# Optimization experiments

Measured on AMD Instinct MI355X. Metric: run time of the kernel, lower is better.

## Reference

```python
import jax, jax.numpy as jnp
import numpy as np

N_NODES = 50000
N_EDGES = 800000
D = 128


def gcn_conv(x, src, dst, W, b, num_nodes):
    # PyG GCNConv: h = X W; add self-loops; symmetric deg^-1/2 normalization; scatter-add; + bias
    h = x @ W                                   # [N, F_out]
    ones = jnp.ones(src.shape[0], dtype=h.dtype)
    deg = jax.ops.segment_sum(ones, dst, num_segments=num_nodes)  # in-degree incl. self-loops
    dinv = jax.lax.rsqrt(jnp.maximum(deg, 1.0))  # deg >= 1 because of self-loops
    norm = dinv[src] * dinv[dst]                 # [E+N]
    msg = h[src] * norm[:, None]                 # gather + scale
    out = jax.ops.segment_sum(msg, dst, num_segments=num_nodes)
    return out + b


def setup_inputs() -> dict:
    key = jax.random.key(0)
    ks = jax.random.split(key, 6)
    x = jax.random.normal(ks[0], (N_NODES, D), dtype=jnp.float32)
    edge_index = jax.random.randint(ks[1], (2, N_EDGES), 0, N_NODES, dtype=jnp.int64)
    s = 1.0 / np.sqrt(D)
    W1 = jax.random.normal(ks[2], (D, D), dtype=jnp.float32) * s
    W2 = jax.random.normal(ks[3], (D, D), dtype=jnp.float32) * s
    Wg = jax.random.normal(ks[4], (2 * D, D), dtype=jnp.float32) * (1.0 / np.sqrt(2 * D))
    b1 = jnp.zeros((D,), jnp.float32)
    b2 = jnp.zeros((D,), jnp.float32)
    bg = jnp.zeros((D,), jnp.float32)
    return {"x": x, "edge_index": edge_index, "W1": W1, "b1": b1,
            "W2": W2, "b2": b2, "Wg": Wg, "bg": bg}


def reference(x, edge_index, W1, b1, W2, b2, Wg, bg):
    num_nodes = x.shape[0]
    x0 = jnp.clip(x, -100.0, 100.0)
    loop = jnp.arange(num_nodes, dtype=edge_index.dtype)
    src = jnp.concatenate([edge_index[0], loop])
    dst = jnp.concatenate([edge_index[1], loop])
    h = jax.nn.relu(gcn_conv(x0, src, dst, W1, b1, num_nodes))
    # F.dropout(p=0.3, training=False) -> identity at inference
    h = jax.nn.relu(gcn_conv(h, src, dst, W2, b2, num_nodes))
    h = h + x0  # residual (out_channels == in_channels)
    gate = jax.nn.sigmoid(jnp.concatenate([h, x0], axis=1) @ Wg + bg)
    return h * gate
```

## Files before the change

### kernel.cpp

```cpp
#include <hip/hip_runtime.h>
#include <hip/hip_bf16.h>

using short8 = __attribute__((ext_vector_type(8))) short;
using f32x4  = __attribute__((ext_vector_type(4))) float;

static constexpr int NN = 50000;
static constexpr int NE = 800000;
static constexpr int MPAD = 50048;
static constexpr int NB2 = 256;
static constexpr int BNODE = 196;
static constexpr int CAPB = 4096;
static constexpr int NCHB = 200;
static constexpr int CHB = NE / NCHB;

__device__ __forceinline__ float clip100(float v) { return fminf(fmaxf(v, -100.f), 100.f); }
__device__ __forceinline__ unsigned short f2b(float v) {
    __hip_bfloat16 h = __float2bfloat16(v);
    return *reinterpret_cast<unsigned short*>(&h);
}
__device__ __forceinline__ float blo(unsigned int u) { return __uint_as_float(u << 16); }
__device__ __forceinline__ float bhi(unsigned int u) { return __uint_as_float(u & 0xFFFF0000u); }
__device__ __forceinline__ float b2f(unsigned short u) {
    return __uint_as_float(((unsigned int)u) << 16);
}

__global__ __launch_bounds__(256) void k_bucket(const int* __restrict__ idx,
                                                int2* __restrict__ epair,
                                                int* __restrict__ gcur) {
    __shared__ int ls[CHB], ld[CHB];
    __shared__ int bcnt[NB2], bb[NB2], bofs[NB2];
    const int tid = threadIdx.x;
    const int beg = blockIdx.x * CHB;
    for (int i = tid; i < CHB; i += 256) {
        ls[i] = idx[beg + i];
        ld[i] = idx[NE + beg + i];
    }
    bcnt[tid] = 0;
    __syncthreads();
    for (int i = tid; i < CHB; i += 256) atomicAdd(&bcnt[ld[i] / BNODE], 1);
    __syncthreads();
    bb[tid] = atomicAdd(&gcur[tid], bcnt[tid]);
    bofs[tid] = 0;
    __syncthreads();
    for (int i = tid; i < CHB; i += 256) {
        const int d = ld[i];
        const int p = d / BNODE;
        const int pos = atomicAdd(&bofs[p], 1);
        epair[p * CAPB + bb[p] + pos] = make_int2(ls[i], d);
    }
}

__global__ __launch_bounds__(256) void k_sortfill(const int2* __restrict__ epair,
                                                  const int* __restrict__ gcur,
                                                  int* __restrict__ rowptr,
                                                  float* __restrict__ dinv,
                                                  int* __restrict__ esrc) {
    __shared__ int ls[CAPB], ld[CAPB], srt[CAPB];
    __shared__ int cntL[256], sc[256], cur[256];
    const int t = threadIdx.x;
    const int b = blockIdx.x;
    sc[t] = gcur[t];
    __syncthreads();
    for (int off = 1; off < 256; off <<= 1) {
        const int add = (t >= off) ? sc[t - off] : 0;
        __syncthreads();
        sc[t] += add;
        __syncthreads();
    }
    const int ne = gcur[b];
    const int base = sc[b] - ne;
    const int nb0 = b * BNODE;
    const int nn = min(NN - nb0, BNODE);
    if (b == 0 && t == 0) rowptr[NN] = NE;

    for (int i = t; i < ne; i += 256) {
        const int2 p = epair[b * CAPB + i];
        ls[i] = p.x;
        ld[i] = p.y - nb0;
    }
    cntL[t] = 0;
    __syncthreads();
    for (int i = t; i < ne; i += 256) atomicAdd(&cntL[ld[i]], 1);
    __syncthreads();
    sc[t] = cntL[t];
    __syncthreads();
    for (int off = 1; off < 256; off <<= 1) {
        const int add = (t >= off) ? sc[t - off] : 0;
        __syncthreads();
        sc[t] += add;
        __syncthreads();
    }
    const int excl = sc[t] - cntL[t];
    cur[t] = excl;
    if (t < nn) {
        rowptr[nb0 + t] = base + excl;
        dinv[nb0 + t] = rsqrtf(1.f + (float)cntL[t]);
    }
    __syncthreads();
    for (int i = t; i < ne; i += 256) {
        const int pos = atomicAdd(&cur[ld[i]], 1);
        srt[pos] = ls[i];
    }
    __syncthreads();
    for (int i = t; i < ne; i += 256) esrc[base + i] = srt[i];
}

__global__ __launch_bounds__(256) void k_cvtw(const float* __restrict__ W1,
                                              const float* __restrict__ W2,
                                              const float* __restrict__ Wg,
                                              unsigned short* __restrict__ Wt1,
                                              unsigned short* __restrict__ Wt2,
                                              unsigned short* __restrict__ Wgt,
                                              int* __restrict__ gcur) {
    const int i = blockIdx.x * 256 + threadIdx.x;
    if (i < NB2) gcur[i] = 0;
    if (i < 16384) {
        const int n = i >> 7, k = i & 127;
        Wt1[i] = f2b(W1[k * 128 + n]);
    } else if (i < 32768) {
        const int j = i - 16384;
        const int n = j >> 7, k = j & 127;
        Wt2[j] = f2b(W2[k * 128 + n]);
    } else {
        const int j = i - 32768;
        const int n = j >> 8, k = j & 255;
        Wgt[j] = f2b(Wg[k * 128 + n]);
    }
}

template <bool AB16>
__global__ __launch_bounds__(256) void k_mfma_lds(const unsigned short* __restrict__ Ab,
                                                  const float* __restrict__ Af,
                                                  const unsigned short* __restrict__ Wt,
                                                  unsigned short* __restrict__ Cb,
                                                  const float* __restrict__ dinv) {
    __shared__ unsigned short wl[128 * 136];
    const int tid = threadIdx.x;
#pragma unroll
    for (int j = tid; j < 2048; j += 256) {
        const int row = j >> 4, c8 = j & 15;
        *(short8*)(wl + row * 136 + c8 * 8) = *(const short8*)(Wt + row * 128 + c8 * 8);
    }
    __syncthreads();

    const int wv = tid >> 6;
    const int ln = tid & 63;
    const int l16 = ln & 15;
    const int qd = ln >> 4;
    const int rowb = blockIdx.x * 64 + wv * 16;
    const long arow = rowb + l16;
    const int kq = qd * 8;

    f32x4 acc[8];
#pragma unroll
    for (int i = 0; i < 8; ++i) acc[i] = (f32x4){0.f, 0.f, 0.f, 0.f};

#pragma unroll
    for (int kc = 0; kc < 4; ++kc) {
        short8 a;
        if (AB16) {
            a = *(const short8*)(Ab + arow * 128 + kc * 32 + kq);
        } else {
            a = (short8){0, 0, 0, 0, 0, 0, 0, 0};
            if (arow < NN) {
                const float* fp = Af + arow * 128 + kc * 32 + kq;
                const float4 f0 = *(const float4*)fp;
                const float4 f1 = *(const float4*)(fp + 4);
                a[0] = (short)f2b(clip100(f0.x));
                a[1] = (short)f2b(clip100(f0.y));
                a[2] = (short)f2b(clip100(f0.z));
                a[3] = (short)f2b(clip100(f0.w));
                a[4] = (short)f2b(clip100(f1.x));
                a[5] = (short)f2b(clip100(f1.y));
                a[6] = (short)f2b(clip100(f1.z));
                a[7] = (short)f2b(clip100(f1.w));
            }
        }
#pragma unroll
        for (int nt = 0; nt < 8; ++nt) {
            const short8 b = *(const short8*)(wl + (nt * 16 + l16) * 136 + kc * 32 + kq);
            acc[nt] = __builtin_amdgcn_mfma_f32_16x16x32_bf16(a, b, acc[nt], 0, 0, 0);
        }
    }

    const int r0 = rowb + qd * 4;
#pragma unroll
    for (int r = 0; r < 4; ++r) {
        const int row = r0 + r;
        if (row < NN) {
            const float dv = dinv[row];
#pragma unroll
            for (int nt = 0; nt < 8; ++nt) {
                Cb[(long)row * 128 + nt * 16 + l16] = f2b(acc[nt][r] * dv);
            }
        }
    }
}

__global__ __launch_bounds__(256) void k_mfma_gate(const unsigned short* __restrict__ Ab,
                                                   const float* __restrict__ Af,
                                                   const unsigned short* __restrict__ Wt,
                                                   const float* __restrict__ bg,
                                                   float* __restrict__ out) {
    __shared__ unsigned short wl[128 * 136];
    const int tid = threadIdx.x;
    const int wv = tid >> 6;
    const int ln = tid & 63;
    const int l16 = ln & 15;
    const int qd = ln >> 4;
    const int rowb = blockIdx.x * 64 + wv * 16;
    const long arow = rowb + l16;
    const int kq = qd * 8;

    f32x4 acc[8];
#pragma unroll
    for (int i = 0; i < 8; ++i) acc[i] = (f32x4){0.f, 0.f, 0.f, 0.f};

#pragma unroll
    for (int j = tid; j < 2048; j += 256) {
        const int row = j >> 4, c8 = j & 15;
        *(short8*)(wl + row * 136 + c8 * 8) = *(const short8*)(Wt + row * 256 + c8 * 8);
    }
    __syncthreads();
    {
        const unsigned short* ap = Ab + arow * 128 + kq;
#pragma unroll
        for (int kc = 0; kc < 4; ++kc) {
            const short8 a = *(const short8*)(ap + kc * 32);
#pragma unroll
            for (int nt = 0; nt < 8; ++nt) {
                const short8 b = *(const short8*)(wl + (nt * 16 + l16) * 136 + kc * 32 + kq);
                acc[nt] = __builtin_amdgcn_mfma_f32_16x16x32_bf16(a, b, acc[nt], 0, 0, 0);
            }
        }
    }
    __syncthreads();

#pragma unroll
    for (int j = tid; j < 2048; j += 256) {
        const int row = j >> 4, c8 = j & 15;
        *(short8*)(wl + row * 136 + c8 * 8) = *(const short8*)(Wt + row * 256 + 128 + c8 * 8);
    }
    __syncthreads();
    {
        const bool valid = arow < NN;
        const float* fp = Af + arow * 128 + kq;
#pragma unroll
        for (int kc = 0; kc < 4; ++kc) {
            short8 a = (short8){0, 0, 0, 0, 0, 0, 0, 0};
            if (valid) {
                const float4 f0 = *(const float4*)(fp + kc * 32);
                const float4 f1 = *(const float4*)(fp + kc * 32 + 4);
                a[0] = (short)f2b(clip100(f0.x));
                a[1] = (short)f2b(clip100(f0.y));
                a[2] = (short)f2b(clip100(f0.z));
                a[3] = (short)f2b(clip100(f0.w));
                a[4] = (short)f2b(clip100(f1.x));
                a[5] = (short)f2b(clip100(f1.y));
                a[6] = (short)f2b(clip100(f1.z));
                a[7] = (short)f2b(clip100(f1.w));
            }
#pragma unroll
            for (int nt = 0; nt < 8; ++nt) {
                const short8 b = *(const short8*)(wl + (nt * 16 + l16) * 136 + kc * 32 + kq);
                acc[nt] = __builtin_amdgcn_mfma_f32_16x16x32_bf16(a, b, acc[nt], 0, 0, 0);
            }
        }
    }

    const int r0 = rowb + qd * 4;
#pragma unroll
    for (int nt = 0; nt < 8; ++nt) {
        const int col = nt * 16 + l16;
        const float bgv = bg[col];
#pragma unroll
        for (int r = 0; r < 4; ++r) {
            const int row = r0 + r;
            if (row < NN) {
                const float g = 1.f / (1.f + __expf(-(acc[nt][r] + bgv)));
                out[(long)row * 128 + col] = b2f(Ab[(long)row * 128 + col]) * g;
            }
        }
    }
}

template <bool RES>
__global__ __launch_bounds__(256) void k_aggr(const unsigned int* __restrict__ As2,
                                              unsigned short* __restrict__ Bb,
                                              const int* __restrict__ rowptr,
                                              const int* __restrict__ esrc,
                                              const float* __restrict__ dinv,
                                              const float* __restrict__ bias,
                                              const float* __restrict__ x) {
    const int d = __builtin_amdgcn_readfirstlane((blockIdx.x * 256 + threadIdx.x) >> 6);
    if (d >= NN) return;
    const int lane = threadIdx.x & 63;
    const float dd = dinv[d];

    const unsigned int u = As2[(long)d * 64 + lane];
    float2 acc;
    acc.x = blo(u);
    acc.y = bhi(u);

    const int beg = rowptr[d];
    const int end = rowptr[d + 1];
    int i = beg;
    for (; i + 8 <= end; i += 8) {
        const int s0 = esrc[i + 0], s1 = esrc[i + 1], s2 = esrc[i + 2], s3 = esrc[i + 3];
        const int s4 = esrc[i + 4], s5 = esrc[i + 5], s6 = esrc[i + 6], s7 = esrc[i + 7];
        const unsigned int v0 = As2[(long)s0 * 64 + lane];
        const unsigned int v1 = As2[(long)s1 * 64 + lane];
        const unsigned int v2 = As2[(long)s2 * 64 + lane];
        const unsigned int v3 = As2[(long)s3 * 64 + lane];
        const unsigned int v4 = As2[(long)s4 * 64 + lane];
        const unsigned int v5 = As2[(long)s5 * 64 + lane];
        const unsigned int v6 = As2[(long)s6 * 64 + lane];
        const unsigned int v7 = As2[(long)s7 * 64 + lane];
        acc.x += ((blo(v0) + blo(v1)) + (blo(v2) + blo(v3))) +
                 ((blo(v4) + blo(v5)) + (blo(v6) + blo(v7)));
        acc.y += ((bhi(v0) + bhi(v1)) + (bhi(v2) + bhi(v3))) +
                 ((bhi(v4) + bhi(v5)) + (bhi(v6) + bhi(v7)));
    }
    if (i + 4 <= end) {
        const int s0 = esrc[i + 0], s1 = esrc[i + 1], s2 = esrc[i + 2], s3 = esrc[i + 3];
        const unsigned int v0 = As2[(long)s0 * 64 + lane];
        const unsigned int v1 = As2[(long)s1 * 64 + lane];
        const unsigned int v2 = As2[(long)s2 * 64 + lane];
        const unsigned int v3 = As2[(long)s3 * 64 + lane];
        acc.x += (blo(v0) + blo(v1)) + (blo(v2) + blo(v3));
        acc.y += (bhi(v0) + bhi(v1)) + (bhi(v2) + bhi(v3));
        i += 4;
    }
    for (; i < end; ++i) {
        const unsigned int v = As2[(long)esrc[i] * 64 + lane];
        acc.x += blo(v);
        acc.y += bhi(v);
    }

    const float2 bv = ((const float2*)bias)[lane];
    acc.x = fmaxf(fmaf(acc.x, dd, bv.x), 0.f);
    acc.y = fmaxf(fmaf(acc.y, dd, bv.y), 0.f);
    if (RES) {
        const float2 xv = ((const float2*)x)[(long)d * 64 + lane];
        acc.x += clip100(xv.x);
        acc.y += clip100(xv.y);
    }
    const unsigned int pack = (unsigned int)f2b(acc.x) | ((unsigned int)f2b(acc.y) << 16);
    ((unsigned int*)Bb)[(long)d * 64 + lane] = pack;
}

extern "C" void kernel_launch(void* const* d_in, const int* in_sizes, int n_in,
                              void* d_out, int out_size, void* d_ws, size_t ws_size,
                              hipStream_t stream) {
    const float* x  = (const float*)d_in[0];
    const int*  eix = (const int*)d_in[1];
    const float* W1 = (const float*)d_in[2];
    const float* b1 = (const float*)d_in[3];
    const float* W2 = (const float*)d_in[4];
    const float* b2 = (const float*)d_in[5];
    const float* Wg = (const float*)d_in[6];
    const float* bg = (const float*)d_in[7];
    float* out = (float*)d_out;

    char* ws = (char*)d_ws;
    unsigned short* As   = (unsigned short*)ws;
    unsigned short* hb   = (unsigned short*)(ws + 12812288);
    unsigned short* Wt1  = (unsigned short*)(ws + 25624576);
    unsigned short* Wt2  = (unsigned short*)(ws + 25657344);
    unsigned short* Wgt  = (unsigned short*)(ws + 25690112);
    int*   rowptr = (int*)(ws + 25755648);
    float* dinv   = (float*)(ws + 25956352);
    int*   gcur   = (int*)(ws + 26157056);
    int*   esrc   = (int*)(ws + 26159104);
    int2*  epair  = (int2*)(ws + 29359104);

    const int ggrid = MPAD / 64;
    dim3 blk(256);

    k_cvtw<<<256, blk, 0, stream>>>(W1, W2, Wg, Wt1, Wt2, Wgt, gcur);
    k_bucket<<<NCHB, blk, 0, stream>>>(eix, epair, gcur);
    k_sortfill<<<NB2, blk, 0, stream>>>(epair, gcur, rowptr, dinv, esrc);

    k_mfma_lds<false><<<ggrid, blk, 0, stream>>>(nullptr, x, Wt1, As, dinv);
    k_aggr<false><<<(NN * 64 + 255) / 256, blk, 0, stream>>>(
        (const unsigned int*)As, hb, rowptr, esrc, dinv, b1, nullptr);

    k_mfma_lds<true><<<ggrid, blk, 0, stream>>>(hb, nullptr, Wt2, As, dinv);
    k_aggr<true><<<(NN * 64 + 255) / 256, blk, 0, stream>>>(
        (const unsigned int*)As, hb, rowptr, esrc, dinv, b2, x);

    k_mfma_gate<<<ggrid, blk, 0, stream>>>(hb, x, Wgt, bg, out);
}
```

Baseline: 213.8 us.

## Fuse preprocessing kernels and overlap CSR build with first GEMM

The weight-conversion kernel is merged with edge bucketing, and the CSR sort/fill kernel is merged with the first X·W1 GEMM into one grid. Those two jobs are picked by block index, so the first GEMM no longer waits for the CSR build. To break the GEMM's dependency on dinv, the source-side degree scaling moves into the first aggregation, which now gathers dinv[src] per edge. This removes kernel launches and serialization gaps. In exchange, layer-1 aggregation does extra per-edge loads and multiplies, and the merged kernel needs more shared memory, which may lower occupancy for its GEMM blocks.

```diff
diff --git a/kernel.cpp b/kernel.cpp
--- a/kernel.cpp
+++ b/kernel.cpp
@@ -24,146 +24,143 @@
     return __uint_as_float(((unsigned int)u) << 16);
 }
 
-__global__ __launch_bounds__(256) void k_bucket(const int* __restrict__ idx,
-                                                int2* __restrict__ epair,
-                                                int* __restrict__ gcur) {
+__global__ __launch_bounds__(256) void k_front(const int* __restrict__ idx,
+                                               int2* __restrict__ epair,
+                                               int* __restrict__ gcur,
+                                               const float* __restrict__ W1,
+                                               const float* __restrict__ W2,
+                                               const float* __restrict__ Wg,
+                                               unsigned short* __restrict__ Wt1,
+                                               unsigned short* __restrict__ Wt2,
+                                               unsigned short* __restrict__ Wgt) {
     __shared__ int ls[CHB], ld[CHB];
     __shared__ int bcnt[NB2], bb[NB2], bofs[NB2];
     const int tid = threadIdx.x;
-    const int beg = blockIdx.x * CHB;
-    for (int i = tid; i < CHB; i += 256) {
-        ls[i] = idx[beg + i];
-        ld[i] = idx[NE + beg + i];
-    }
-    bcnt[tid] = 0;
-    __syncthreads();
-    for (int i = tid; i < CHB; i += 256) atomicAdd(&bcnt[ld[i] / BNODE], 1);
-    __syncthreads();
-    bb[tid] = atomicAdd(&gcur[tid], bcnt[tid]);
-    bofs[tid] = 0;
-    __syncthreads();
-    for (int i = tid; i < CHB; i += 256) {
-        const int d = ld[i];
-        const int p = d / BNODE;
-        const int pos = atomicAdd(&bofs[p], 1);
-        epair[p * CAPB + bb[p] + pos] = make_int2(ls[i], d);
-    }
-}
-
-__global__ __launch_bounds__(256) void k_sortfill(const int2* __restrict__ epair,
-                                                  const int* __restrict__ gcur,
-                                                  int* __restrict__ rowptr,
-                                                  float* __restrict__ dinv,
-                                                  int* __restrict__ esrc) {
-    __shared__ int ls[CAPB], ld[CAPB], srt[CAPB];
-    __shared__ int cntL[256], sc[256], cur[256];
-    const int t = threadIdx.x;
-    const int b = blockIdx.x;
-    sc[t] = gcur[t];
-    __syncthreads();
-    for (int off = 1; off < 256; off <<= 1) {
-        const int add = (t >= off) ? sc[t - off] : 0;
-        __syncthreads();
-        sc[t] += add;
-        __syncthreads();
-    }
-    const int ne = gcur[b];
-    const int base = sc[b] - ne;
-    const int nb0 = b * BNODE;
-    const int nn = min(NN - nb0, BNODE);
-    if (b == 0 && t == 0) rowptr[NN] = NE;
-
-    for (int i = t; i < ne; i += 256) {
-        const int2 p = epair[b * CAPB + i];
-        ls[i] = p.x;
-        ld[i] = p.y - nb0;
-    }
-    cntL[t] = 0;
-    __syncthreads();
-    for (int i = t; i < ne; i += 256) atomicAdd(&cntL[ld[i]], 1);
-    __syncthreads();
-    sc[t] = cntL[t];
-    __syncthreads();
-    for (int off = 1; off < 256; off <<= 1) {
-        const int add = (t >= off) ? sc[t - off] : 0;
-        __syncthreads();
-        sc[t] += add;
-        __syncthreads();
-    }
-    const int excl = sc[t] - cntL[t];
-    cur[t] = excl;
-    if (t < nn) {
-        rowptr[nb0 + t] = base + excl;
-        dinv[nb0 + t] = rsqrtf(1.f + (float)cntL[t]);
-    }
-    __syncthreads();
-    for (int i = t; i < ne; i += 256) {
-        const int pos = atomicAdd(&cur[ld[i]], 1);
-        srt[pos] = ls[i];
-    }
-    __syncthreads();
-    for (int i = t; i < ne; i += 256) esrc[base + i] = srt[i];
-}
-
-__global__ __launch_bounds__(256) void k_cvtw(const float* __restrict__ W1,
-                                              const float* __restrict__ W2,
-                                              const float* __restrict__ Wg,
-                                              unsigned short* __restrict__ Wt1,
-                                              unsigned short* __restrict__ Wt2,
-                                              unsigned short* __restrict__ Wgt,
-                                              int* __restrict__ gcur) {
-    const int i = blockIdx.x * 256 + threadIdx.x;
-    if (i < NB2) gcur[i] = 0;
-    if (i < 16384) {
-        const int n = i >> 7, k = i & 127;
-        Wt1[i] = f2b(W1[k * 128 + n]);
-    } else if (i < 32768) {
-        const int j = i - 16384;
-        const int n = j >> 7, k = j & 127;
-        Wt2[j] = f2b(W2[k * 128 + n]);
+    if (blockIdx.x < NCHB) {
+        const int beg = blockIdx.x * CHB;
+        for (int i = tid; i < CHB; i += 256) {
+            ls[i] = idx[beg + i];
+            ld[i] = idx[NE + beg + i];
+        }
+        bcnt[tid] = 0;
+        __syncthreads();
+        for (int i = tid; i < CHB; i += 256) atomicAdd(&bcnt[ld[i] / BNODE], 1);
+        __syncthreads();
+        bb[tid] = atomicAdd(&gcur[tid], bcnt[tid]);
+        bofs[tid] = 0;
+        __syncthreads();
+        for (int i = tid; i < CHB; i += 256) {
+            const int d = ld[i];
+            const int p = d / BNODE;
+            const int pos = atomicAdd(&bofs[p], 1);
+            epair[p * CAPB + bb[p] + pos] = make_int2(ls[i], d);
+        }
     } else {
-        const int j = i - 32768;
-        const int n = j >> 8, k = j & 255;
-        Wgt[j] = f2b(Wg[k * 128 + n]);
-    }
-}
-
-template <bool AB16>
-__global__ __launch_bounds__(256) void k_mfma_lds(const unsigned short* __restrict__ Ab,
-                                                  const float* __restrict__ Af,
-                                                  const unsigned short* __restrict__ Wt,
-                                                  unsigned short* __restrict__ Cb,
-                                                  const float* __restrict__ dinv) {
-    __shared__ unsigned short wl[128 * 136];
+        const int i = (blockIdx.x - NCHB) * 256 + tid;
+        if (i < 16384) {
+            const int n = i >> 7, k = i & 127;
+            Wt1[i] = f2b(W1[k * 128 + n]);
+        } else if (i < 32768) {
+            const int j = i - 16384;
+            const int n = j >> 7, k = j & 127;
+            Wt2[j] = f2b(W2[k * 128 + n]);
+        } else {
+            const int j = i - 32768;
+            const int n = j >> 8, k = j & 255;
+            Wgt[j] = f2b(Wg[k * 128 + n]);
+        }
+    }
+}
+
+__global__ __launch_bounds__(256) void k_mid(const int2* __restrict__ epair,
+                                             const int* __restrict__ gcur,
+                                             int* __restrict__ rowptr,
+                                             float* __restrict__ dinv,
+                                             int* __restrict__ esrc,
+                                             const float* __restrict__ x,
+                                             const unsigned short* __restrict__ Wt,
+                                             unsigned short* __restrict__ Cb) {
+    __shared__ alignas(16) char smem[CAPB * 3 * 4 + 3 * 256 * 4];
     const int tid = threadIdx.x;
-#pragma unroll
-    for (int j = tid; j < 2048; j += 256) {
-        const int row = j >> 4, c8 = j & 15;
-        *(short8*)(wl + row * 136 + c8 * 8) = *(const short8*)(Wt + row * 128 + c8 * 8);
-    }
-    __syncthreads();
-
-    const int wv = tid >> 6;
-    const int ln = tid & 63;
-    const int l16 = ln & 15;
-    const int qd = ln >> 4;
-    const int rowb = blockIdx.x * 64 + wv * 16;
-    const long arow = rowb + l16;
-    const int kq = qd * 8;
-
-    f32x4 acc[8];
-#pragma unroll
-    for (int i = 0; i < 8; ++i) acc[i] = (f32x4){0.f, 0.f, 0.f, 0.f};
-
-#pragma unroll
-    for (int kc = 0; kc < 4; ++kc) {
-        short8 a;
-        if (AB16) {
-            a = *(const short8*)(Ab + arow * 128 + kc * 32 + kq);
-        } else {
-            a = (short8){0, 0, 0, 0, 0, 0, 0, 0};
+    if (blockIdx.x < NB2) {
+        int* ls   = (int*)smem;
+        int* ld   = ls + CAPB;
+        int* srt  = ld + CAPB;
+        int* cntL = srt + CAPB;
+        int* sc   = cntL + 256;
+        int* cur  = sc + 256;
+        const int t = tid;
+        const int b = blockIdx.x;
+        sc[t] = gcur[t];
+        __syncthreads();
+        for (int off = 1; off < 256; off <<= 1) {
+            const int add = (t >= off) ? sc[t - off] : 0;
+            __syncthreads();
+            sc[t] += add;
+            __syncthreads();
+        }
+        const int ne = gcur[b];
+        const int base = sc[b] - ne;
+        const int nb0 = b * BNODE;
+        const int nn = min(NN - nb0, BNODE);
+        if (b == 0 && t == 0) rowptr[NN] = NE;
+
+        for (int i = t; i < ne; i += 256) {
+            const int2 p = epair[b * CAPB + i];
+            ls[i] = p.x;
+            ld[i] = p.y - nb0;
+        }
+        cntL[t] = 0;
+        __syncthreads();
+        for (int i = t; i < ne; i += 256) atomicAdd(&cntL[ld[i]], 1);
+        __syncthreads();
+        sc[t] = cntL[t];
+        __syncthreads();
+        for (int off = 1; off < 256; off <<= 1) {
+            const int add = (t >= off) ? sc[t - off] : 0;
+            __syncthreads();
+            sc[t] += add;
+            __syncthreads();
+        }
+        const int excl = sc[t] - cntL[t];
+        cur[t] = excl;
+        if (t < nn) {
+            rowptr[nb0 + t] = base + excl;
+            dinv[nb0 + t] = rsqrtf(1.f + (float)cntL[t]);
+        }
+        __syncthreads();
+        for (int i = t; i < ne; i += 256) {
+            const int pos = atomicAdd(&cur[ld[i]], 1);
+            srt[pos] = ls[i];
+        }
+        __syncthreads();
+        for (int i = t; i < ne; i += 256) esrc[base + i] = srt[i];
+    } else {
+        unsigned short* wl = (unsigned short*)smem;
+#pragma unroll
+        for (int j = tid; j < 2048; j += 256) {
+            const int row = j >> 4, c8 = j & 15;
+            *(short8*)(wl + row * 136 + c8 * 8) = *(const short8*)(Wt + row * 128 + c8 * 8);
+        }
+        __syncthreads();
+
+        const int wv = tid >> 6;
+        const int ln = tid & 63;
+        const int l16 = ln & 15;
+        const int qd = ln >> 4;
+        const int rowb = (blockIdx.x - NB2) * 64 + wv * 16;
+        const long arow = rowb + l16;
+        const int kq = qd * 8;
+
+        f32x4 acc[8];
+#pragma unroll
+        for (int i = 0; i < 8; ++i) acc[i] = (f32x4){0.f, 0.f, 0.f, 0.f};
+
+#pragma unroll
+        for (int kc = 0; kc < 4; ++kc) {
+            short8 a = (short8){0, 0, 0, 0, 0, 0, 0, 0};
             if (arow < NN) {
-                const float* fp = Af + arow * 128 + kc * 32 + kq;
+                const float* fp = x + arow * 128 + kc * 32 + kq;
                 const float4 f0 = *(const float4*)fp;
                 const float4 f1 = *(const float4*)(fp + 4);
                 a[0] = (short)f2b(clip100(f0.x));
@@ -175,7 +172,55 @@
                 a[6] = (short)f2b(clip100(f1.z));
                 a[7] = (short)f2b(clip100(f1.w));
             }
-        }
+#pragma unroll
+            for (int nt = 0; nt < 8; ++nt) {
+                const short8 b = *(const short8*)(wl + (nt * 16 + l16) * 136 + kc * 32 + kq);
+                acc[nt] = __builtin_amdgcn_mfma_f32_16x16x32_bf16(a, b, acc[nt], 0, 0, 0);
+            }
+        }
+
+        const int r0 = rowb + qd * 4;
+#pragma unroll
+        for (int r = 0; r < 4; ++r) {
+            const int row = r0 + r;
+            if (row < NN) {
+#pragma unroll
+                for (int nt = 0; nt < 8; ++nt) {
+                    Cb[(long)row * 128 + nt * 16 + l16] = f2b(acc[nt][r]);
+                }
+            }
+        }
+    }
+}
+
+__global__ __launch_bounds__(256) void k_mfma2(const unsigned short* __restrict__ Ab,
+                                               const unsigned short* __restrict__ Wt,
+                                               unsigned short* __restrict__ Cb,
+                                               const float* __restrict__ dinv) {
+    __shared__ unsigned short wl[128 * 136];
+    const int tid = threadIdx.x;
+#pragma unroll
+    for (int j = tid; j < 2048; j += 256) {
+        const int row = j >> 4, c8 = j & 15;
+        *(short8*)(wl + row * 136 + c8 * 8) = *(const short8*)(Wt + row * 128 + c8 * 8);
+    }
+    __syncthreads();
+
+    const int wv = tid >> 6;
+    const int ln = tid & 63;
+    const int l16 = ln & 15;
+    const int qd = ln >> 4;
+    const int rowb = blockIdx.x * 64 + wv * 16;
+    const long arow = rowb + l16;
+    const int kq = qd * 8;
+
+    f32x4 acc[8];
+#pragma unroll
+    for (int i = 0; i < 8; ++i) acc[i] = (f32x4){0.f, 0.f, 0.f, 0.f};
+
+#pragma unroll
+    for (int kc = 0; kc < 4; ++kc) {
+        const short8 a = *(const short8*)(Ab + arow * 128 + kc * 32 + kq);
 #pragma unroll
         for (int nt = 0; nt < 8; ++nt) {
             const short8 b = *(const short8*)(wl + (nt * 16 + l16) * 136 + kc * 32 + kq);
@@ -284,7 +329,7 @@
     }
 }
 
-template <bool RES>
+template <bool RES, bool ESCALE>
 __global__ __launch_bounds__(256) void k_aggr(const unsigned int* __restrict__ As2,
                                               unsigned short* __restrict__ Bb,
                                               const int* __restrict__ rowptr,
@@ -299,8 +344,13 @@
 
     const unsigned int u = As2[(long)d * 64 + lane];
     float2 acc;
-    acc.x = blo(u);
-    acc.y = bhi(u);
+    if (ESCALE) {
+        acc.x = blo(u) * dd;
+        acc.y = bhi(u) * dd;
+    } else {
+        acc.x = blo(u);
+        acc.y = bhi(u);
+    }
 
     const int beg = rowptr[d];
     const int end = rowptr[d + 1];
@@ -316,10 +366,19 @@
         const unsigned int v5 = As2[(long)s5 * 64 + lane];
         const unsigned int v6 = As2[(long)s6 * 64 + lane];
         const unsigned int v7 = As2[(long)s7 * 64 + lane];
-        acc.x += ((blo(v0) + blo(v1)) + (blo(v2) + blo(v3))) +
-                 ((blo(v4) + blo(v5)) + (blo(v6) + blo(v7)));
-        acc.y += ((bhi(v0) + bhi(v1)) + (bhi(v2) + bhi(v3))) +
-                 ((bhi(v4) + bhi(v5)) + (bhi(v6) + bhi(v7)));
+        if (ESCALE) {
+            const float w0 = dinv[s0], w1 = dinv[s1], w2 = dinv[s2], w3 = dinv[s3];
+            const float w4 = dinv[s4], w5 = dinv[s5], w6 = dinv[s6], w7 = dinv[s7];
+            acc.x += ((blo(v0) * w0 + blo(v1) * w1) + (blo(v2) * w2 + blo(v3) * w3)) +
+                     ((blo(v4) * w4 + blo(v5) * w5) + (blo(v6) * w6 + blo(v7) * w7));
+            acc.y += ((bhi(v0) * w0 + bhi(v1) * w1) + (bhi(v2) * w2 + bhi(v3) * w3)) +
+                     ((bhi(v4) * w4 + bhi(v5) * w5) + (bhi(v6) * w6 + bhi(v7) * w7));
+        } else {
+            acc.x += ((blo(v0) + blo(v1)) + (blo(v2) + blo(v3))) +
+                     ((blo(v4) + blo(v5)) + (blo(v6) + blo(v7)));
+            acc.y += ((bhi(v0) + bhi(v1)) + (bhi(v2) + bhi(v3))) +
+                     ((bhi(v4) + bhi(v5)) + (bhi(v6) + bhi(v7)));
+        }
     }
     if (i + 4 <= end) {
         const int s0 = esrc[i + 0], s1 = esrc[i + 1], s2 = esrc[i + 2], s3 = esrc[i + 3];
@@ -327,14 +386,27 @@
         const unsigned int v1 = As2[(long)s1 * 64 + lane];
         const unsigned int v2 = As2[(long)s2 * 64 + lane];
         const unsigned int v3 = As2[(long)s3 * 64 + lane];
-        acc.x += (blo(v0) + blo(v1)) + (blo(v2) + blo(v3));
-        acc.y += (bhi(v0) + bhi(v1)) + (bhi(v2) + bhi(v3));
+        if (ESCALE) {
+            const float w0 = dinv[s0], w1 = dinv[s1], w2 = dinv[s2], w3 = dinv[s3];
+            acc.x += (blo(v0) * w0 + blo(v1) * w1) + (blo(v2) * w2 + blo(v3) * w3);
+            acc.y += (bhi(v0) * w0 + bhi(v1) * w1) + (bhi(v2) * w2 + bhi(v3) * w3);
+        } else {
+            acc.x += (blo(v0) + blo(v1)) + (blo(v2) + blo(v3));
+            acc.y += (bhi(v0) + bhi(v1)) + (bhi(v2) + bhi(v3));
+        }
         i += 4;
     }
     for (; i < end; ++i) {
-        const unsigned int v = As2[(long)esrc[i] * 64 + lane];
-        acc.x += blo(v);
-        acc.y += bhi(v);
+        const int s = esrc[i];
+        const unsigned int v = As2[(long)s * 64 + lane];
+        if (ESCALE) {
+            const float w = dinv[s];
+            acc.x = fmaf(blo(v), w, acc.x);
+            acc.y = fmaf(bhi(v), w, acc.y);
+        } else {
+            acc.x += blo(v);
+            acc.y += bhi(v);
+        }
     }
 
     const float2 bv = ((const float2*)bias)[lane];
@@ -377,16 +449,18 @@
     const int ggrid = MPAD / 64;
     dim3 blk(256);
 
-    k_cvtw<<<256, blk, 0, stream>>>(W1, W2, Wg, Wt1, Wt2, Wgt, gcur);
-    k_bucket<<<NCHB, blk, 0, stream>>>(eix, epair, gcur);
-    k_sortfill<<<NB2, blk, 0, stream>>>(epair, gcur, rowptr, dinv, esrc);
-
-    k_mfma_lds<false><<<ggrid, blk, 0, stream>>>(nullptr, x, Wt1, As, dinv);
-    k_aggr<false><<<(NN * 64 + 255) / 256, blk, 0, stream>>>(
+    hipMemsetAsync(gcur, 0, NB2 * sizeof(int), stream);
+
+    k_front<<<NCHB + 256, blk, 0, stream>>>(eix, epair, gcur, W1, W2, Wg, Wt1, Wt2, Wgt);
+
+    k_mid<<<NB2 + ggrid, blk, 0, stream>>>(epair, gcur, rowptr, dinv, esrc, x, Wt1, As);
+
+    k_aggr<false, true><<<(NN * 64 + 255) / 256, blk, 0, stream>>>(
         (const unsigned int*)As, hb, rowptr, esrc, dinv, b1, nullptr);
 
-    k_mfma_lds<true><<<ggrid, blk, 0, stream>>>(hb, nullptr, Wt2, As, dinv);
-    k_aggr<true><<<(NN * 64 + 255) / 256, blk, 0, stream>>>(
+    k_mfma2<<<ggrid, blk, 0, stream>>>(hb, Wt2, As, dinv);
+
+    k_aggr<true, false><<<(NN * 64 + 255) / 256, blk, 0, stream>>>(
         (const unsigned int*)As, hb, rowptr, esrc, dinv, b2, x);
 
     k_mfma_gate<<<ggrid, blk, 0, stream>>>(hb, x, Wgt, bg, out);
```

Result: no change. 213.5 us (-0.2%).
